# Performance work log

Measured on AMD Instinct MI355X. Metric: run time of the kernel, lower is better.

The kernel has to match this reference:

```python
import jax, jax.numpy as jnp
import numpy as np

B, C, H, W = 4, 3, 1024, 1024
EPS = 1e-8


def setup_inputs() -> dict:
    key = jax.random.key(0)
    k1, k2 = jax.random.split(key)
    im0 = jax.random.normal(k1, (B, C, H, W), dtype=jnp.float32)
    # grid = identity pixel mesh + small random water-distortion displacement
    yy, xx = jnp.meshgrid(jnp.arange(H, dtype=jnp.float32),
                          jnp.arange(W, dtype=jnp.float32), indexing='ij')
    base = jnp.stack([xx, yy], axis=-1)  # [H,W,2] in (x,y) order
    disp = 2.0 * jax.random.normal(k2, (B, H, W, 2), dtype=jnp.float32)
    grid = base[None] + disp  # [B,H,W,2]
    return {"im0": im0, "grid": grid}


def reference(im0, grid):
    """Forward splatting (griddata): scatter im0 values at coordinates `grid`
    onto the regular HxW grid with bilinear weights, normalized by the
    accumulated weight at each cell."""
    b, c, h, w = im0.shape
    n = h * w
    x = grid[..., 0].reshape(b, n)
    y = grid[..., 1].reshape(b, n)
    x0f = jnp.floor(x)
    y0f = jnp.floor(y)
    dx = x - x0f  # bilinear fractions (differentiable w.r.t. grid)
    dy = y - y0f
    x0 = x0f.astype(jnp.int32)
    y0 = y0f.astype(jnp.int32)

    # 4 corner indices [b,4,n] and bilinear weights
    xs = jnp.stack([x0, x0 + 1, x0, x0 + 1], axis=1)
    ys = jnp.stack([y0, y0, y0 + 1, y0 + 1], axis=1)
    ws = jnp.stack([(1 - dx) * (1 - dy), dx * (1 - dy),
                    (1 - dx) * dy, dx * dy], axis=1)
    valid = (xs >= 0) & (xs < w) & (ys >= 0) & (ys < h)
    ws = ws * valid.astype(ws.dtype)
    idx = (jnp.clip(ys, 0, h - 1) * w + jnp.clip(xs, 0, w - 1)).reshape(b, 4 * n)
    ws = ws.reshape(b, 4 * n)

    vals = im0.reshape(b, c, n)
    contrib = (vals[:, :, None, :] * ws.reshape(b, 1, 4, n)).reshape(b, c, 4 * n)

    def splat(v, wgt, i):
        den = jnp.zeros((n,), wgt.dtype).at[i].add(wgt)
        num = jnp.zeros((c, n), v.dtype).at[:, i].add(v)
        return num / jnp.maximum(den, EPS)[None, :]

    out = jax.vmap(splat)(contrib, ws, idx)  # [b,c,n]
    return out.reshape(b, c, h, w)
```

## Files before the change

### kernel.cpp

```cpp
#include <hip/hip_runtime.h>
#include <hip/hip_fp16.h>

#define B 4
#define C 3
#define H 1024
#define W 1024
#define N (H * W)
#define EPS 1e-8f

#define TW 32
#define TH 32
#define R 8
#define WIN 48
#define NSRC (WIN * WIN)
#define NTASKS (NSRC / 4)
#define BDIM 33
#define NBINS (BDIM * BDIM)
#define NBINW ((NBINS + 1) / 2)
#define K 5
#define NTX (W / TW)
#define NTY (H / TH)
#define NTILES (NTX * NTY * B)

struct OutlierRec { int idx; float dw, d0, d1, d2; };

__global__ __launch_bounds__(256, 4) void splat_gather(
    const float* __restrict__ im0,
    const float* __restrict__ grid,
    float* __restrict__ out,
    float* __restrict__ den,
    int* __restrict__ tileCnt,
    OutlierRec* __restrict__ recs,
    int slots)
{
    __shared__ unsigned recW0[NSRC];
    __shared__ unsigned recW1[NSRC];
    __shared__ unsigned recW2[NSRC];
    __shared__ unsigned binCntP[NBINW];
    __shared__ unsigned short ent[K * NBINS];

    const int bid = blockIdx.x;
    const int b = bid >> 10;
    const int t = bid & 1023;
    const int tx0 = (t & (NTX - 1)) * TW;
    const int ty0 = (t >> 5) * TH;
    const int tid = threadIdx.x;

    for (int i = tid; i < NBINW; i += 256) binCntP[i] = 0u;
    __syncthreads();

    const int lx0 = tx0 - R;
    const int ly0 = ty0 - R;

    const float* imb   = im0 + (size_t)b * C * N;
    const float* gbase = grid + (size_t)b * N * 2;

    auto push_rec = [&](int xi, int yi, float w, float v0, float v1, float v2) {
        const int tile = (b << 10) | ((yi >> 5) << 5) | (xi >> 5);
        const int slot = atomicAdd(&tileCnt[tile], 1);
        if (slot < slots) {
            OutlierRec r;
            r.idx = b * N + yi * W + xi;
            r.dw = w; r.d0 = v0 * w; r.d1 = v1 * w; r.d2 = v2 * w;
            recs[(size_t)tile * slots + slot] = r;
        }
    };

    for (int task = tid; task < NTASKS; task += 256) {
        const int row = task / (WIN / 4);
        const int col = (task - row * (WIN / 4)) * 4;
        const int sy = ly0 + row;
        const int sxg = lx0 + col;
        if ((unsigned)sy >= H || (unsigned)sxg >= W) continue;

        const int n = sy * W + sxg;
        const float4 g0 = *(const float4*)(gbase + 2 * n);
        const float4 g1 = *(const float4*)(gbase + 2 * n + 4);
        const float4 c0 = *(const float4*)(imb + n);
        const float4 c1 = *(const float4*)(imb + N + n);
        const float4 c2 = *(const float4*)(imb + 2 * N + n);

        const float gxk[4] = {g0.x, g0.z, g1.x, g1.z};
        const float gyk[4] = {g0.y, g0.w, g1.y, g1.w};
        const float v0k[4] = {c0.x, c0.y, c0.z, c0.w};
        const float v1k[4] = {c1.x, c1.y, c1.z, c1.w};
        const float v2k[4] = {c2.x, c2.y, c2.z, c2.w};

#pragma unroll
        for (int k = 0; k < 4; ++k) {
            const int sx = sxg + k;
            const int i = k * NTASKS + task;
            const float gx = gxk[k], gy = gyk[k];
            const float x0f = floorf(gx);
            const float y0f = floorf(gy);
            const float dx = gx - x0f;
            const float dy = gy - y0f;
            const int x0 = (int)x0f;
            const int y0 = (int)y0f;

            {
                unsigned dq = (unsigned)(dx * 65536.0f);
                unsigned eq = (unsigned)(dy * 65536.0f);
                if (dq > 65535u) dq = 65535u;
                if (eq > 65535u) eq = 65535u;
                recW0[i] = dq | (eq << 16);
                __half2 h01 = __floats2half2_rn(v0k[k], v1k[k]);
                recW1[i] = *(unsigned*)&h01;
                __half2 h2 = __floats2half2_rn(v2k[k], 0.f);
                recW2[i] = *(unsigned*)&h2;
            }

            const int bx = x0 - tx0 + 1;
            const int by = y0 - ty0 + 1;
            if ((unsigned)bx < BDIM && (unsigned)by < BDIM) {
                const int bin = by * BDIM + bx;
                const unsigned sh = (unsigned)(bin & 1) * 16u;
                const unsigned old = atomicAdd(&binCntP[bin >> 1], 1u << sh);
                const unsigned slot = (old >> sh) & 0xffffu;
                if (slot < K) {
                    ent[slot * NBINS + bin] = (unsigned short)i;
                } else {
                    const float wxa[2] = {1.f - dx, dx};
                    const float wya[2] = {1.f - dy, dy};
#pragma unroll
                    for (int cy2 = 0; cy2 < 2; ++cy2)
#pragma unroll
                        for (int cx2 = 0; cx2 < 2; ++cx2) {
                            const int xi = x0 + cx2, yi = y0 + cy2;
                            if ((unsigned)(xi - tx0) < TW &&
                                (unsigned)(yi - ty0) < TH)
                                push_rec(xi, yi, wxa[cx2] * wya[cy2],
                                         v0k[k], v1k[k], v2k[k]);
                        }
                }
            }

            if ((unsigned)(sx - tx0) < TW && (unsigned)(sy - ty0) < TH) {
                const float wxa[2] = {1.f - dx, dx};
                const float wya[2] = {1.f - dy, dy};
#pragma unroll
                for (int cy2 = 0; cy2 < 2; ++cy2)
#pragma unroll
                    for (int cx2 = 0; cx2 < 2; ++cx2) {
                        const int xi = x0 + cx2, yi = y0 + cy2;
                        if ((unsigned)xi < W && (unsigned)yi < H) {
                            const int ox0 = (xi >> 5) << 5;
                            const int oy0 = (yi >> 5) << 5;
                            const bool covered =
                                (sx >= ox0 - R) && (sx < ox0 + TW + R) &&
                                (sy >= oy0 - R) && (sy < oy0 + TH + R);
                            if (!covered)
                                push_rec(xi, yi, wxa[cx2] * wya[cy2],
                                         v0k[k], v1k[k], v2k[k]);
                        }
                    }
            }
        }
    }
    __syncthreads();

    const int cx = tid & 31;
    const int ry = (tid >> 5) * 4;
    float* outb = out + (size_t)b * C * N;
    float* denb = den + (size_t)b * N;

    float d[4]  = {0.f, 0.f, 0.f, 0.f};
    float a0[4] = {0.f, 0.f, 0.f, 0.f};
    float a1[4] = {0.f, 0.f, 0.f, 0.f};
    float a2[4] = {0.f, 0.f, 0.f, 0.f};

#pragma unroll
    for (int s = 0; s < 5; ++s) {
        const int by = ry + s;
#pragma unroll
        for (int jx = 0; jx < 2; ++jx) {
            const int bx = cx + jx;
            const int bin = by * BDIM + bx;
            const unsigned cw = binCntP[bin >> 1];
            const int cnt = min((int)((cw >> ((unsigned)(bin & 1) * 16u)) & 0xffffu), K);
            for (int e = 0; e < cnt; ++e) {
                const int i = ent[e * NBINS + bin];
                const unsigned w0 = recW0[i];
                const unsigned uv01 = recW1[i];
                const unsigned uv2 = recW2[i];
                const float dx = (float)(w0 & 0xffffu) * (1.f / 65536.f);
                const float dy = (float)(w0 >> 16) * (1.f / 65536.f);
                const float2 v01 = __half22float2(*(const __half2*)&uv01);
                const float v2 = __half2float(((const __half2*)&uv2)->x);
                const float wx = jx ? (1.f - dx) : dx;
                if (s > 0) {
                    const float w = wx * (1.f - dy);
                    d[s - 1] += w;
                    a0[s - 1] += v01.x * w;
                    a1[s - 1] += v01.y * w;
                    a2[s - 1] += v2 * w;
                }
                if (s < 4) {
                    const float w = wx * dy;
                    d[s] += w;
                    a0[s] += v01.x * w;
                    a1[s] += v01.y * w;
                    a2[s] += v2 * w;
                }
            }
        }
    }

#pragma unroll
    for (int s = 0; s < 4; ++s) {
        const float inv = 1.f / fmaxf(d[s], EPS);
        const int gi = (ty0 + ry + s) * W + tx0 + cx;
        denb[gi] = d[s];
        outb[gi]         = a0[s] * inv;
        outb[N + gi]     = a1[s] * inv;
        outb[2 * N + gi] = a2[s] * inv;
    }
}

__global__ __launch_bounds__(64) void fix_tiles(
    float* __restrict__ out,
    float* __restrict__ den,
    const int* __restrict__ tileCnt,
    const OutlierRec* __restrict__ recs,
    int slots)
{
    const int bid = blockIdx.x;
    int cnt = tileCnt[bid];
    if (cnt <= 0) return;
    cnt = min(cnt, slots);
    const int tid = threadIdx.x;
    if (tid >= cnt) return;

    OutlierRec rec = recs[(size_t)bid * slots + tid];
    float dw = rec.dw, d0 = rec.d0, d1 = rec.d1, d2 = rec.d2;
    bool first = true;
    for (int r2 = 0; r2 < cnt; ++r2) {
        if (r2 == tid) continue;
        OutlierRec o = recs[(size_t)bid * slots + r2];
        if (o.idx == rec.idx) {
            if (r2 < tid) { first = false; break; }
            dw += o.dw; d0 += o.d0; d1 += o.d1; d2 += o.d2;
        }
    }
    if (!first) return;

    const int b = rec.idx >> 20;
    const int cell = rec.idx & (N - 1);
    float* outb = out + (size_t)b * C * N + cell;
    float* dptr = den + ((size_t)b << 20) + cell;

    float d = *dptr;
    const float m = fmaxf(d, EPS);
    float n0 = outb[0] * m;
    float n1 = outb[N] * m;
    float n2 = outb[2 * N] * m;
    d += dw; n0 += d0; n1 += d1; n2 += d2;
    const float inv = 1.f / fmaxf(d, EPS);
    *dptr = d;
    outb[0]     = n0 * inv;
    outb[N]     = n1 * inv;
    outb[2 * N] = n2 * inv;
}

extern "C" void kernel_launch(void* const* d_in, const int* in_sizes, int n_in,
                              void* d_out, int out_size, void* d_ws, size_t ws_size,
                              hipStream_t stream) {
    const float* im0 = (const float*)d_in[0];
    const float* grid = (const float*)d_in[1];
    float* out = (float*)d_out;

    int* tileCnt = (int*)d_ws;
    float* den = (float*)((char*)d_ws + 16384);
    const size_t rec_off = 16384 + (size_t)B * N * sizeof(float);
    OutlierRec* recs = (OutlierRec*)((char*)d_ws + rec_off);
    int slots = 0;
    if (ws_size > rec_off) {
        size_t avail = (ws_size - rec_off) / sizeof(OutlierRec);
        slots = (int)(avail / NTILES);
        if (slots > 32) slots = 32;
    }

    (void)hipMemsetAsync(tileCnt, 0, NTILES * sizeof(int), stream);

    splat_gather<<<NTILES, 256, 0, stream>>>(im0, grid, out, den,
                                             tileCnt, recs, slots);
    fix_tiles<<<NTILES, 64, 0, stream>>>(out, den, tileCnt, recs, slots);
}
```

Before: 171.8 us.

## Replace fixed-capacity bin slots with counting-sort binning via prefix scan

Source points are now binned with a two-pass counting sort. A first pass counts points per bin, a block-wide prefix scan turns the counts into offsets, and a second pass writes records compactly in bin order. This removes the fixed K-slot entry table and the indirect index lookup, lets the gather walk one contiguous range per pair of adjacent bins, and stores the third channel as a 16-bit half to shrink LDS. The smaller LDS footprint allows raising the occupancy hint from 4 to 6 blocks per CU. The cost is a second read of the grid, extra atomics and two more barriers, and the overflow outlier path for crowded bins is no longer taken.

```diff
diff --git a/kernel.cpp b/kernel.cpp
--- a/kernel.cpp
+++ b/kernel.cpp
@@ -17,14 +17,13 @@
 #define BDIM 33
 #define NBINS (BDIM * BDIM)
 #define NBINW ((NBINS + 1) / 2)
-#define K 5
 #define NTX (W / TW)
 #define NTY (H / TH)
 #define NTILES (NTX * NTY * B)
 
 struct OutlierRec { int idx; float dw, d0, d1, d2; };
 
-__global__ __launch_bounds__(256, 4) void splat_gather(
+__global__ __launch_bounds__(256, 6) void splat_gather(
     const float* __restrict__ im0,
     const float* __restrict__ grid,
     float* __restrict__ out,
@@ -35,9 +34,9 @@
 {
     __shared__ unsigned recW0[NSRC];
     __shared__ unsigned recW1[NSRC];
-    __shared__ unsigned recW2[NSRC];
+    __shared__ unsigned short recV2[NSRC];
     __shared__ unsigned binCntP[NBINW];
-    __shared__ unsigned short ent[K * NBINS];
+    __shared__ int wtot[4];
 
     const int bid = blockIdx.x;
     const int b = bid >> 10;
@@ -76,6 +75,70 @@
         const int n = sy * W + sxg;
         const float4 g0 = *(const float4*)(gbase + 2 * n);
         const float4 g1 = *(const float4*)(gbase + 2 * n + 4);
+        const float gxk[4] = {g0.x, g0.z, g1.x, g1.z};
+        const float gyk[4] = {g0.y, g0.w, g1.y, g1.w};
+#pragma unroll
+        for (int k = 0; k < 4; ++k) {
+            const int x0 = (int)floorf(gxk[k]);
+            const int y0 = (int)floorf(gyk[k]);
+            const int bx = x0 - tx0 + 1;
+            const int by = y0 - ty0 + 1;
+            if ((unsigned)bx < BDIM && (unsigned)by < BDIM) {
+                const int bin = by * BDIM + bx;
+                atomicAdd(&binCntP[bin >> 1], 1u << ((unsigned)(bin & 1) * 16u));
+            }
+        }
+    }
+    __syncthreads();
+
+    {
+        int c[6] = {0, 0, 0, 0, 0, 0};
+        const int w0 = tid * 3;
+        const bool act = (tid * 6) < NBINS;
+        if (act) {
+#pragma unroll
+            for (int j = 0; j < 3; ++j) {
+                const int w = w0 + j;
+                const unsigned wv = (w < NBINW) ? binCntP[w] : 0u;
+                c[2 * j]     = (int)(wv & 0xffffu);
+                c[2 * j + 1] = (int)(wv >> 16);
+            }
+        }
+        const int tsum = c[0] + c[1] + c[2] + c[3] + c[4] + c[5];
+        int x = tsum;
+#pragma unroll
+        for (int off = 1; off < 64; off <<= 1) {
+            const int y = __shfl_up(x, off);
+            if ((tid & 63) >= off) x += y;
+        }
+        if ((tid & 63) == 63) wtot[tid >> 6] = x;
+        __syncthreads();
+        int ex = x - tsum;
+        for (int i = 0; i < (tid >> 6); ++i) ex += wtot[i];
+        if (act) {
+#pragma unroll
+            for (int j = 0; j < 3; ++j) {
+                const int w = w0 + j;
+                if (w < NBINW) {
+                    const unsigned lo = (unsigned)ex; ex += c[2 * j];
+                    const unsigned hi = (unsigned)ex; ex += c[2 * j + 1];
+                    binCntP[w] = (lo & 0xffffu) | (hi << 16);
+                }
+            }
+        }
+    }
+    __syncthreads();
+
+    for (int task = tid; task < NTASKS; task += 256) {
+        const int row = task / (WIN / 4);
+        const int col = (task - row * (WIN / 4)) * 4;
+        const int sy = ly0 + row;
+        const int sxg = lx0 + col;
+        if ((unsigned)sy >= H || (unsigned)sxg >= W) continue;
+
+        const int n = sy * W + sxg;
+        const float4 g0 = *(const float4*)(gbase + 2 * n);
+        const float4 g1 = *(const float4*)(gbase + 2 * n + 4);
         const float4 c0 = *(const float4*)(imb + n);
         const float4 c1 = *(const float4*)(imb + N + n);
         const float4 c2 = *(const float4*)(imb + 2 * N + n);
@@ -89,7 +152,6 @@
 #pragma unroll
         for (int k = 0; k < 4; ++k) {
             const int sx = sxg + k;
-            const int i = k * NTASKS + task;
             const float gx = gxk[k], gy = gyk[k];
             const float x0f = floorf(gx);
             const float y0f = floorf(gy);
@@ -98,41 +160,21 @@
             const int x0 = (int)x0f;
             const int y0 = (int)y0f;
 
-            {
-                unsigned dq = (unsigned)(dx * 65536.0f);
-                unsigned eq = (unsigned)(dy * 65536.0f);
-                if (dq > 65535u) dq = 65535u;
-                if (eq > 65535u) eq = 65535u;
-                recW0[i] = dq | (eq << 16);
-                __half2 h01 = __floats2half2_rn(v0k[k], v1k[k]);
-                recW1[i] = *(unsigned*)&h01;
-                __half2 h2 = __floats2half2_rn(v2k[k], 0.f);
-                recW2[i] = *(unsigned*)&h2;
-            }
-
             const int bx = x0 - tx0 + 1;
             const int by = y0 - ty0 + 1;
             if ((unsigned)bx < BDIM && (unsigned)by < BDIM) {
                 const int bin = by * BDIM + bx;
                 const unsigned sh = (unsigned)(bin & 1) * 16u;
                 const unsigned old = atomicAdd(&binCntP[bin >> 1], 1u << sh);
-                const unsigned slot = (old >> sh) & 0xffffu;
-                if (slot < K) {
-                    ent[slot * NBINS + bin] = (unsigned short)i;
-                } else {
-                    const float wxa[2] = {1.f - dx, dx};
-                    const float wya[2] = {1.f - dy, dy};
-#pragma unroll
-                    for (int cy2 = 0; cy2 < 2; ++cy2)
-#pragma unroll
-                        for (int cx2 = 0; cx2 < 2; ++cx2) {
-                            const int xi = x0 + cx2, yi = y0 + cy2;
-                            if ((unsigned)(xi - tx0) < TW &&
-                                (unsigned)(yi - ty0) < TH)
-                                push_rec(xi, yi, wxa[cx2] * wya[cy2],
-                                         v0k[k], v1k[k], v2k[k]);
-                        }
-                }
+                const int slot = (int)((old >> sh) & 0xffffu);
+                unsigned dq = (unsigned)(dx * 65536.0f);
+                unsigned eq = (unsigned)(dy * 65536.0f);
+                if (dq > 65535u) dq = 65535u;
+                if (eq > 65535u) eq = 65535u;
+                recW0[slot] = dq | (eq << 16);
+                __half2 h01 = __floats2half2_rn(v0k[k], v1k[k]);
+                recW1[slot] = *(unsigned*)&h01;
+                recV2[slot] = __half_as_ushort(__float2half_rn(v2k[k]));
             }
 
             if ((unsigned)(sx - tx0) < TW && (unsigned)(sy - ty0) < TH) {
@@ -164,6 +206,11 @@
     float* outb = out + (size_t)b * C * N;
     float* denb = den + (size_t)b * N;
 
+    auto END = [&](int bb) -> int {
+        const unsigned wv = binCntP[bb >> 1];
+        return (int)((wv >> ((unsigned)(bb & 1) * 16u)) & 0xffffu);
+    };
+
     float d[4]  = {0.f, 0.f, 0.f, 0.f};
     float a0[4] = {0.f, 0.f, 0.f, 0.f};
     float a1[4] = {0.f, 0.f, 0.f, 0.f};
@@ -172,36 +219,31 @@
 #pragma unroll
     for (int s = 0; s < 5; ++s) {
         const int by = ry + s;
-#pragma unroll
-        for (int jx = 0; jx < 2; ++jx) {
-            const int bx = cx + jx;
-            const int bin = by * BDIM + bx;
-            const unsigned cw = binCntP[bin >> 1];
-            const int cnt = min((int)((cw >> ((unsigned)(bin & 1) * 16u)) & 0xffffu), K);
-            for (int e = 0; e < cnt; ++e) {
-                const int i = ent[e * NBINS + bin];
-                const unsigned w0 = recW0[i];
-                const unsigned uv01 = recW1[i];
-                const unsigned uv2 = recW2[i];
-                const float dx = (float)(w0 & 0xffffu) * (1.f / 65536.f);
-                const float dy = (float)(w0 >> 16) * (1.f / 65536.f);
-                const float2 v01 = __half22float2(*(const __half2*)&uv01);
-                const float v2 = __half2float(((const __half2*)&uv2)->x);
-                const float wx = jx ? (1.f - dx) : dx;
-                if (s > 0) {
-                    const float w = wx * (1.f - dy);
-                    d[s - 1] += w;
-                    a0[s - 1] += v01.x * w;
-                    a1[s - 1] += v01.y * w;
-                    a2[s - 1] += v2 * w;
-                }
-                if (s < 4) {
-                    const float w = wx * dy;
-                    d[s] += w;
-                    a0[s] += v01.x * w;
-                    a1[s] += v01.y * w;
-                    a2[s] += v2 * w;
-                }
+        const int bin0 = by * BDIM + cx;
+        const int e0 = (bin0 == 0) ? 0 : END(bin0 - 1);
+        const int m  = END(bin0);
+        const int e1 = END(bin0 + 1);
+        for (int e = e0; e < e1; ++e) {
+            const unsigned w0 = recW0[e];
+            const unsigned uv01 = recW1[e];
+            const float dx = (float)(w0 & 0xffffu) * (1.f / 65536.f);
+            const float dy = (float)(w0 >> 16) * (1.f / 65536.f);
+            const float2 v01 = __half22float2(*(const __half2*)&uv01);
+            const float v2 = __half2float(__ushort_as_half(recV2[e]));
+            const float wx = (e < m) ? dx : (1.f - dx);
+            if (s > 0) {
+                const float w = wx * (1.f - dy);
+                d[s - 1] += w;
+                a0[s - 1] += v01.x * w;
+                a1[s - 1] += v01.y * w;
+                a2[s - 1] += v2 * w;
+            }
+            if (s < 4) {
+                const float w = wx * dy;
+                d[s] += w;
+                a0[s] += v01.x * w;
+                a1[s] += v01.y * w;
+                a2[s] += v2 * w;
             }
         }
     }
```

New measurement: 160.2 us. 1.07x faster.
